# Performance work log

Hardware: AMD Instinct MI355X
Metric: run time of the kernel (lower is better)

## Reference

```python
import jax, jax.numpy as jnp
import numpy as np

# libmolgrid GridMaker defaults (gnina): resolution 0.5 A, dimension 23.5 A
RES = 0.5
DIM = 23.5
G = int(round(DIM / RES)) + 1  # 48 grid points per axis
N_ATOMS = 800
N_TYPES = 28  # gnina default atom typing


def setup_inputs() -> dict:
    key = jax.random.key(0)
    k1, k2, k3 = jax.random.split(key, 3)
    # atoms spread around the grid center (grid spans +-11.75 A)
    coords = jax.random.normal(k1, (N_ATOMS, 3), dtype=jnp.float32) * 4.0
    # continuous (soft) type vectors in [0,1)
    types = jax.random.uniform(k2, (N_ATOMS, N_TYPES), dtype=jnp.float32)
    # van-der-Waals-like radii in [1.0, 1.8) A
    radii = 1.0 + 0.8 * jax.random.uniform(k3, (N_ATOMS,), dtype=jnp.float32)
    center = jnp.zeros((3,), dtype=jnp.float32)
    return {"center": center, "coords": coords, "types": types, "radii": radii}


def _density(coords, radii, center):
    """Per-atom libmolgrid density on the [G,G,G] grid -> [N,G,G,G].

    f(d) = exp(-2 d^2/r^2)                         for d <  r
         = e^-2 (4 (d/r)^2 - 12 (d/r) + 9)          for r <= d < 1.5 r
         = 0                                        otherwise
    (C1-continuous quadratic tail, libmolgrid defaults grm=1.0, final=1.5).
    """
    origin = center - DIM / 2.0  # [3]
    ax = jnp.arange(G, dtype=jnp.float32) * RES  # [G]
    dx = (origin[0] + ax)[None, :] - coords[:, 0:1]  # [N,G]
    dy = (origin[1] + ax)[None, :] - coords[:, 1:2]
    dz = (origin[2] + ax)[None, :] - coords[:, 2:3]
    d2 = (dx[:, :, None, None] ** 2
          + dy[:, None, :, None] ** 2
          + dz[:, None, None, :] ** 2)  # [N,G,G,G]
    r = radii[:, None, None, None]
    dr2 = d2 / (r * r)
    dr = jnp.sqrt(jnp.maximum(dr2, 1e-12))
    gauss = jnp.exp(-2.0 * dr2)
    inv_e2 = jnp.float32(np.exp(-2.0))
    quad = inv_e2 * (4.0 * dr2 - 12.0 * dr + 9.0)
    return jnp.where(dr < 1.0, gauss, jnp.where(dr < 1.5, quad, 0.0))


def reference(center, coords, types, radii):
    dens = _density(coords, radii, center)  # [N,G,G,G]
    # weight each atom's footprint by its type vector and scatter-sum over atoms
    return jnp.einsum('nxyz,nt->txyz', dens, types)  # [T,G,G,G]
```

## Files before the change

### kernel.cpp

```cpp
#include <hip/hip_runtime.h>

#define GR    48
#define GR2   (GR * GR)
#define GR3   (GR * GR * GR)
#define NA    800
#define NT    28
#define RESF  0.5f
#define HALF_DIM 11.75f
#define INV_E2 0.13533528323661270f

#define TXC   2
#define TYC   2
#define TZC   16
#define NTX   (GR / TXC)
#define NTY   (GR / TYC)
#define NTZ   (GR / TZC)
#define NBLK  (NTX * NTY * NTZ)
#define KB    64
#define TSL   8

__global__ __launch_bounds__(256) void c2g_kernel(
    const float* __restrict__ center,
    const float* __restrict__ coords,
    const float* __restrict__ types,
    const float* __restrict__ radii,
    float* __restrict__ out)
{
    __shared__ float s_ax[NA], s_ay[NA], s_az[NA], s_ir2[NA];
    __shared__ int   s_ai[NA];
    __shared__ int   s_cnt;
    __shared__ float s_val[KB * 64];
    __shared__ float s_tb[KB * 32];

    const int tid  = threadIdx.x;
    const int lane = tid & 63;
    const int w    = tid >> 6;
    const int b    = blockIdx.x;
    const int tz   = b % NTZ;
    const int ty   = (b / NTZ) % NTY;
    const int tx   = b / (NTZ * NTY);

    const float ox = center[0] - HALF_DIM;
    const float oy = center[1] - HALF_DIM;
    const float oz = center[2] - HALF_DIM;

    const float bxlo = ox + tx * (TXC * RESF), bxhi = bxlo + (TXC - 1) * RESF;
    const float bylo = oy + ty * (TYC * RESF), byhi = bylo + (TYC - 1) * RESF;
    const float bzlo = oz + tz * (TZC * RESF), bzhi = bzlo + (TZC - 1) * RESF;

    if (tid == 0) s_cnt = 0;
    __syncthreads();

    for (int a0 = 0; a0 < NA; a0 += 256) {
        int a = a0 + tid;
        bool accept = false;
        float ax = 0.f, ay = 0.f, az = 0.f, r = 1.f;
        if (a < NA) {
            ax = coords[3 * a + 0];
            ay = coords[3 * a + 1];
            az = coords[3 * a + 2];
            r  = radii[a];
            float cut = 1.5f * r;
            float ddx = ax - fminf(fmaxf(ax, bxlo), bxhi);
            float ddy = ay - fminf(fmaxf(ay, bylo), byhi);
            float ddz = az - fminf(fmaxf(az, bzlo), bzhi);
            float d2 = fmaf(ddx, ddx, fmaf(ddy, ddy, ddz * ddz));
            accept = d2 < cut * cut;
        }
        unsigned long long m = __ballot(accept);
        if (m) {
            int base = 0;
            if (lane == 0) base = atomicAdd(&s_cnt, __popcll(m));
            base = __shfl(base, 0);
            if (accept) {
                int p = base + __popcll(m & ((1ull << lane) - 1ull));
                s_ax[p] = ax; s_ay[p] = ay; s_az[p] = az;
                s_ir2[p] = 1.0f / (r * r);
                s_ai[p] = a;
            }
        }
    }
    __syncthreads();
    const int cnt = s_cnt;

    const int lzz = lane & 15;
    const int ly2 = (lane >> 4) & 1;
    const int lx2 = lane >> 5;
    const float gx = bxlo + lx2 * RESF;
    const float gy = bylo + ly2 * RESF;
    const float gz = bzlo + lzz * RESF;

    float acc[TSL];
    #pragma unroll
    for (int j = 0; j < TSL; ++j) acc[j] = 0.0f;
    const int tbase = w * TSL;

    for (int k0 = 0; k0 < cnt; k0 += KB) {
        const int kmax = (cnt - k0 < KB) ? (cnt - k0) : KB;

        float4 tv0 = make_float4(0.f, 0.f, 0.f, 0.f);
        float4 tv1 = tv0;
        {
            int s = tid;
            int row = s >> 3, q = s & 7;
            if (q < 7 && row < kmax)
                tv0 = *(const float4*)(types + s_ai[k0 + row] * NT + q * 4);
            s = tid + 256;
            row = s >> 3; q = s & 7;
            if (q < 7 && row < kmax)
                tv1 = *(const float4*)(types + s_ai[k0 + row] * NT + q * 4);
        }

        #pragma unroll
        for (int j = 0; j < 16; ++j) {
            int row = w * 16 + j;
            float val = 0.0f;
            if (row < kmax) {
                int k = k0 + row;
                float dx = gx - s_ax[k];
                float dy = gy - s_ay[k];
                float dz = gz - s_az[k];
                float d2 = fmaf(dx, dx, fmaf(dy, dy, dz * dz));
                float dr2 = d2 * s_ir2[k];
                float g  = __expf(-2.0f * dr2);
                float dr = sqrtf(dr2);
                float q  = INV_E2 * fmaf(4.0f, dr2, fmaf(-12.0f, dr, 9.0f));
                val = (dr2 < 1.0f) ? g : ((dr2 < 2.25f) ? q : 0.0f);
            }
            s_val[row * 64 + lane] = val;
        }

        {
            int s = tid;
            *(float4*)&s_tb[(s >> 3) * 32 + (s & 7) * 4] = tv0;
            s = tid + 256;
            *(float4*)&s_tb[(s >> 3) * 32 + (s & 7) * 4] = tv1;
        }
        __syncthreads();

        #pragma unroll 4
        for (int k = 0; k < kmax; ++k) {
            float v = s_val[k * 64 + lane];
            const float* tr = &s_tb[k * 32 + tbase];
            #pragma unroll
            for (int j = 0; j < TSL; ++j)
                acc[j] = fmaf(v, tr[j], acc[j]);
        }
        __syncthreads();
    }

    const int gidx = (tx * TXC + lx2) * GR2 + (ty * TYC + ly2) * GR + tz * TZC + lzz;
    #pragma unroll
    for (int j = 0; j < TSL; ++j) {
        int t = tbase + j;
        if (t < NT) out[t * GR3 + gidx] = acc[j];
    }
}

extern "C" void kernel_launch(void* const* d_in, const int* in_sizes, int n_in,
                              void* d_out, int out_size, void* d_ws, size_t ws_size,
                              hipStream_t stream) {
    const float* center = (const float*)d_in[0];
    const float* coords = (const float*)d_in[1];
    const float* types  = (const float*)d_in[2];
    const float* radii  = (const float*)d_in[3];
    float* out = (float*)d_out;

    c2g_kernel<<<dim3(NBLK), dim3(256), 0, stream>>>(center, coords, types, radii, out);
}
```

Before: 74.40 us.

## Use bf16 MFMA for density-by-type contraction with staged output transpose

Replaces the per-lane scalar FMA reduction over atoms and types with bf16 16x16x32 MFMA instructions. Densities and type weights are rounded to bf16 and stored in padded shared-memory tiles, and atom data is packed into a float4 per atom. Results pass through a shared-memory transpose before coalesced global stores. The aim is to offload the inner contraction to matrix cores, at the cost of bf16 rounding error in the accumulated sums.

```diff
diff --git a/kernel.cpp b/kernel.cpp
--- a/kernel.cpp
+++ b/kernel.cpp
@@ -17,7 +17,16 @@
 #define NTZ   (GR / TZC)
 #define NBLK  (NTX * NTY * NTZ)
 #define KB    64
-#define TSL   8
+#define KPAD  80
+
+typedef __attribute__((ext_vector_type(8))) short short8;
+typedef __attribute__((ext_vector_type(4))) float floatx4;
+
+__device__ inline unsigned short f2bf(float x) {
+    unsigned u = __builtin_bit_cast(unsigned, x);
+    u = (u + 0x7FFFu + ((u >> 16) & 1u)) >> 16;
+    return (unsigned short)u;
+}
 
 __global__ __launch_bounds__(256) void c2g_kernel(
     const float* __restrict__ center,
@@ -26,11 +35,12 @@
     const float* __restrict__ radii,
     float* __restrict__ out)
 {
-    __shared__ float s_ax[NA], s_ay[NA], s_az[NA], s_ir2[NA];
-    __shared__ int   s_ai[NA];
-    __shared__ int   s_cnt;
-    __shared__ float s_val[KB * 64];
-    __shared__ float s_tb[KB * 32];
+    __shared__ float4 s_atom[NA];
+    __shared__ int    s_ai[NA];
+    __shared__ int    s_cnt;
+    __shared__ unsigned short s_val[64 * KPAD];
+    __shared__ unsigned short s_tT[32 * KPAD];
+    __shared__ float  s_out[64 * 33];
 
     const int tid  = threadIdx.x;
     const int lane = tid & 63;
@@ -74,8 +84,7 @@
             base = __shfl(base, 0);
             if (accept) {
                 int p = base + __popcll(m & ((1ull << lane) - 1ull));
-                s_ax[p] = ax; s_ay[p] = ay; s_az[p] = az;
-                s_ir2[p] = 1.0f / (r * r);
+                s_atom[p] = make_float4(ax, ay, az, 1.0f / (r * r));
                 s_ai[p] = a;
             }
         }
@@ -90,70 +99,91 @@
     const float gy = bylo + ly2 * RESF;
     const float gz = bzlo + lzz * RESF;
 
-    float acc[TSL];
-    #pragma unroll
-    for (int j = 0; j < TSL; ++j) acc[j] = 0.0f;
-    const int tbase = w * TSL;
+    const int lm = lane & 15;
+    const int lg = lane >> 4;
+
+    floatx4 acc0 = {0.f, 0.f, 0.f, 0.f};
+    floatx4 acc1 = {0.f, 0.f, 0.f, 0.f};
+
+    const int r0 = tid >> 3,         q0 = tid & 7;
+    const int r1 = (tid + 256) >> 3, q1 = tid & 7;
 
     for (int k0 = 0; k0 < cnt; k0 += KB) {
         const int kmax = (cnt - k0 < KB) ? (cnt - k0) : KB;
 
         float4 tv0 = make_float4(0.f, 0.f, 0.f, 0.f);
         float4 tv1 = tv0;
+        if (q0 < 7 && r0 < kmax)
+            tv0 = *(const float4*)(types + s_ai[k0 + r0] * NT + q0 * 4);
+        if (q1 < 7 && r1 < kmax)
+            tv1 = *(const float4*)(types + s_ai[k0 + r1] * NT + q1 * 4);
+
+        unsigned pk[8];
+        #pragma unroll
+        for (int jj = 0; jj < 8; ++jj) {
+            float v[2];
+            #pragma unroll
+            for (int h = 0; h < 2; ++h) {
+                int row = w * 16 + 2 * jj + h;
+                float vv = 0.0f;
+                if (row < kmax) {
+                    float4 at = s_atom[k0 + row];
+                    float dx = gx - at.x;
+                    float dy = gy - at.y;
+                    float dz = gz - at.z;
+                    float d2 = fmaf(dx, dx, fmaf(dy, dy, dz * dz));
+                    float dr2 = d2 * at.w;
+                    float g  = __expf(-2.0f * dr2);
+                    float dr = sqrtf(dr2);
+                    float q  = INV_E2 * fmaf(4.0f, dr2, fmaf(-12.0f, dr, 9.0f));
+                    vv = (dr2 < 1.0f) ? g : ((dr2 < 2.25f) ? q : 0.0f);
+                }
+                v[h] = vv;
+            }
+            pk[jj] = (unsigned)f2bf(v[0]) | ((unsigned)f2bf(v[1]) << 16);
+        }
+        *(uint4*)&s_val[lane * KPAD + w * 16]     = *(uint4*)&pk[0];
+        *(uint4*)&s_val[lane * KPAD + w * 16 + 8] = *(uint4*)&pk[4];
+
         {
-            int s = tid;
-            int row = s >> 3, q = s & 7;
-            if (q < 7 && row < kmax)
-                tv0 = *(const float4*)(types + s_ai[k0 + row] * NT + q * 4);
-            s = tid + 256;
-            row = s >> 3; q = s & 7;
-            if (q < 7 && row < kmax)
-                tv1 = *(const float4*)(types + s_ai[k0 + row] * NT + q * 4);
-        }
+            const float* e0 = &tv0.x;
+            const float* e1 = &tv1.x;
+            #pragma unroll
+            for (int i = 0; i < 4; ++i) {
+                s_tT[(q0 * 4 + i) * KPAD + r0] = f2bf(e0[i]);
+                s_tT[(q1 * 4 + i) * KPAD + r1] = f2bf(e1[i]);
+            }
+        }
+        __syncthreads();
 
         #pragma unroll
-        for (int j = 0; j < 16; ++j) {
-            int row = w * 16 + j;
-            float val = 0.0f;
-            if (row < kmax) {
-                int k = k0 + row;
-                float dx = gx - s_ax[k];
-                float dy = gy - s_ay[k];
-                float dz = gz - s_az[k];
-                float d2 = fmaf(dx, dx, fmaf(dy, dy, dz * dz));
-                float dr2 = d2 * s_ir2[k];
-                float g  = __expf(-2.0f * dr2);
-                float dr = sqrtf(dr2);
-                float q  = INV_E2 * fmaf(4.0f, dr2, fmaf(-12.0f, dr, 9.0f));
-                val = (dr2 < 1.0f) ? g : ((dr2 < 2.25f) ? q : 0.0f);
-            }
-            s_val[row * 64 + lane] = val;
-        }
-
-        {
-            int s = tid;
-            *(float4*)&s_tb[(s >> 3) * 32 + (s & 7) * 4] = tv0;
-            s = tid + 256;
-            *(float4*)&s_tb[(s >> 3) * 32 + (s & 7) * 4] = tv1;
+        for (int ks = 0; ks < 2; ++ks) {
+            int ko = ks * 32 + lg * 8;
+            short8 afr = *(const short8*)&s_val[(w * 16 + lm) * KPAD + ko];
+            short8 b0  = *(const short8*)&s_tT[lm * KPAD + ko];
+            short8 b1  = *(const short8*)&s_tT[(16 + lm) * KPAD + ko];
+            acc0 = __builtin_amdgcn_mfma_f32_16x16x32_bf16(afr, b0, acc0, 0, 0, 0);
+            acc1 = __builtin_amdgcn_mfma_f32_16x16x32_bf16(afr, b1, acc1, 0, 0, 0);
         }
         __syncthreads();
-
-        #pragma unroll 4
-        for (int k = 0; k < kmax; ++k) {
-            float v = s_val[k * 64 + lane];
-            const float* tr = &s_tb[k * 32 + tbase];
-            #pragma unroll
-            for (int j = 0; j < TSL; ++j)
-                acc[j] = fmaf(v, tr[j], acc[j]);
-        }
-        __syncthreads();
-    }
-
-    const int gidx = (tx * TXC + lx2) * GR2 + (ty * TYC + ly2) * GR + tz * TZC + lzz;
+    }
+
     #pragma unroll
-    for (int j = 0; j < TSL; ++j) {
-        int t = tbase + j;
-        if (t < NT) out[t * GR3 + gidx] = acc[j];
+    for (int r = 0; r < 4; ++r) {
+        int cellO = w * 16 + lg * 4 + r;
+        s_out[cellO * 33 + lm]      = acc0[r];
+        s_out[cellO * 33 + 16 + lm] = acc1[r];
+    }
+    __syncthreads();
+
+    #pragma unroll
+    for (int i = 0; i < 7; ++i) {
+        int idx = i * 256 + tid;
+        int t = idx >> 6;
+        int c = idx & 63;
+        int z = c & 15, y = (c >> 4) & 1, x = c >> 5;
+        int gidx = (tx * TXC + x) * GR2 + (ty * TYC + y) * GR + tz * TZC + z;
+        out[t * GR3 + gidx] = s_out[c * 33 + t];
     }
 }
 
```

Result: faster. 72.06 us (-3.1%).
